# Optimization experiments

Hardware: AMD Instinct MI355X
Metric: run time of the kernel (lower is better)

Reference implementation:

```python
import jax, jax.numpy as jnp
import numpy as np
from jax import lax

B, T, D, K = 2, 4096, 128, 256


def setup_inputs() -> dict:
    key = jax.random.key(0)
    ks = jax.random.split(key, 5)
    s = 0.05
    return {
        "z": jax.random.normal(ks[0], (B, T, D), jnp.float32),
        "conv_kernel": jax.random.normal(ks[1], (K, 1, D), jnp.float32) * s,  # flax WIO depthwise
        "conv_bias": jnp.zeros((D,), jnp.float32),
        "Wq": jax.random.normal(ks[2], (D, D), jnp.float32) * s,
        "bq": jnp.zeros((D,), jnp.float32),
        "Wk": jax.random.normal(ks[3], (D, D), jnp.float32) * s,
        "bk": jnp.zeros((D,), jnp.float32),
        "Wo": jax.random.normal(ks[4], (D, D), jnp.float32) * s,
        "bo": jnp.zeros((D,), jnp.float32),
    }


def _sphere_norm(x):
    return x / jnp.maximum(jnp.linalg.norm(x, axis=-1, keepdims=True), 1e-8)


def reference(z, conv_kernel, conv_bias, Wq, bq, Wk, bk, Wo, bo):
    Bv, Tv, Dv = z.shape
    Kv = conv_kernel.shape[0]

    # Depthwise causal memory conv (flax nn.Conv, padding='CAUSAL', groups=D)
    memory_force = lax.conv_general_dilated(
        z, conv_kernel, window_strides=(1,), padding=[(Kv - 1, 0)],
        dimension_numbers=("NWC", "WIO", "NWC"), feature_group_count=Dv,
    ) + conv_bias

    # Keys are computed from the base point z once, shared across RK4 stages
    k_hat = _sphere_norm(z @ Wk + bk)  # [B,T,D]
    mask = jnp.tril(jnp.ones((Tv, Tv), z.dtype))  # causal mask

    def vector_field(z_curr):
        q_hat = _sphere_norm(z_curr @ Wq + bq)
        dots = jnp.einsum("btd,bsd->bts", q_hat, k_hat)  # [B,T,T]
        attn = jnp.sin(dots) * mask  # Kuramoto-style sin coupling, causal
        kuramoto = jnp.einsum("bts,bsd->btd", attn, k_hat) @ Wo + bo
        total = memory_force + kuramoto
        # project to tangent space of the sphere at z_curr
        return total - jnp.sum(total * z_curr, axis=-1, keepdims=True) * z_curr

    h = 1.0

    def retract(z_base, v):
        return _sphere_norm(z_base + v)

    k1 = vector_field(z)
    k2 = vector_field(retract(z, 0.5 * h * k1))
    k3 = vector_field(retract(z, 0.5 * h * k2))
    k4 = vector_field(retract(z, h * k3))
    v_final = (h / 6.0) * (k1 + 2 * k2 + 2 * k3 + k4)
    return retract(z, v_final)
```

## Files before the change

kernel.cpp:

```cpp
#include <hip/hip_runtime.h>
#include <hip/hip_bf16.h>

#define BB 2
#define TT 4096
#define DD 128
#define KK 256
#define NROW (BB*TT)
#define NELT (NROW*DD)

typedef _Float16 f16;
typedef __attribute__((ext_vector_type(8))) f16 half8;
typedef __attribute__((ext_vector_type(2))) __fp16 fp16x2;
typedef __attribute__((ext_vector_type(4))) float f32x4;
typedef __attribute__((ext_vector_type(16))) float f32x16;
typedef __attribute__((ext_vector_type(2))) int i32x2;
typedef __attribute__((ext_vector_type(4))) int i32x4;

__device__ __forceinline__ int pack2(float a, float b){
  fp16x2 h = __builtin_amdgcn_cvt_pkrtz(a, b);
  return __builtin_bit_cast(int, h);
}

__device__ __forceinline__ void stage_w_f16(int tid, const float* __restrict__ W, f16* Wh){
  #pragma unroll
  for (int it = 0; it < 8; it++){
    int idx = tid + it*256;
    f32x4 a = *(const f32x4*)(W + (size_t)idx*8);
    f32x4 b = *(const f32x4*)(W + (size_t)idx*8 + 4);
    half8 h;
    #pragma unroll
    for (int u = 0; u < 4; u++){ h[u] = (f16)a[u]; h[4+u] = (f16)b[u]; }
    *(half8*)(Wh + (size_t)idx*8) = h;
  }
}

__device__ __forceinline__ void proj_norm_rows(
    int tid, int r0,
    const float* __restrict__ src, const float* __restrict__ W, const float* __restrict__ bias,
    f16* __restrict__ dst, f16* __restrict__ dstT)
{
  __shared__ f16 Wh[DD*DD];
  __shared__ float zs[32*DD];
  stage_w_f16(tid, W, Wh);
  #pragma unroll
  for (int it = 0; it < 4; it++){
    int idx = tid + it*256;
    *(f32x4*)(zs + idx*4) = *(const f32x4*)(src + (size_t)r0*DD + idx*4);
  }
  __syncthreads();
  int c = tid & 15, rr = tid >> 4;
  float acc0[8], acc1[8];
  #pragma unroll
  for (int u = 0; u < 8; u++){ float bv = bias[c*8+u]; acc0[u] = bv; acc1[u] = bv; }
  const float* zr0 = zs + rr*DD;
  const float* zr1 = zs + (rr+16)*DD;
  #pragma unroll 4
  for (int i = 0; i < DD; i++){
    half8 wv = *(const half8*)(Wh + i*DD + c*8);
    float a0 = zr0[i], a1 = zr1[i];
    #pragma unroll
    for (int u = 0; u < 8; u++){
      float w = (float)wv[u];
      acc0[u] = fmaf(a0, w, acc0[u]);
      acc1[u] = fmaf(a1, w, acc1[u]);
    }
  }
  float s0 = 0.f, s1 = 0.f;
  #pragma unroll
  for (int u = 0; u < 8; u++){ s0 = fmaf(acc0[u], acc0[u], s0); s1 = fmaf(acc1[u], acc1[u], s1); }
  #pragma unroll
  for (int m = 1; m < 16; m <<= 1){ s0 += __shfl_xor(s0, m, 16); s1 += __shfl_xor(s1, m, 16); }
  float inv0 = 1.f / fmaxf(sqrtf(s0), 1e-8f);
  float inv1 = 1.f / fmaxf(sqrtf(s1), 1e-8f);
  half8 h0, h1;
  #pragma unroll
  for (int u = 0; u < 8; u++){ h0[u] = (f16)(acc0[u]*inv0); h1[u] = (f16)(acc1[u]*inv1); }
  int row0 = r0 + rr, row1 = row0 + 16;
  *(half8*)(dst + (size_t)row0*DD + c*8) = h0;
  *(half8*)(dst + (size_t)row1*DD + c*8) = h1;
  if (dstT){
    int b = row0 >> 12, t0 = row0 & 4095, t1 = row1 & 4095;
    #pragma unroll
    for (int u = 0; u < 8; u++){
      dstT[((size_t)b*DD + c*8 + u)*TT + t0] = h0[u];
      dstT[((size_t)b*DD + c*8 + u)*TT + t1] = h1[u];
    }
  }
}

__global__ __launch_bounds__(256) void k_prep(
    const float* __restrict__ z, const float* __restrict__ Wk, const float* __restrict__ bk,
    const float* __restrict__ ck, const float* __restrict__ cb,
    const float* __restrict__ Wq, const float* __restrict__ bq,
    f16* __restrict__ khb, f16* __restrict__ khT, f16* __restrict__ qhb,
    float* __restrict__ mf)
{
  int tid = threadIdx.x;
  if (blockIdx.x < 512){
    int bid = blockIdx.x;
    int d = tid & 127, tg = tid >> 7;
    int b = bid >> 8;
    int tbase = ((bid & 255) << 4) + tg*8;
    const float* zb = z + (size_t)b*TT*DD;
    float acc[8];
    #pragma unroll
    for (int j = 0; j < 8; j++) acc[j] = 0.f;
    float ckq[8];
    #pragma unroll
    for (int u = 0; u < 8; u++) ckq[u] = 0.f;
    int sstart = tbase - (KK-1);
    for (int ch = 0; ch < 33; ch++){
      #pragma unroll
      for (int u = 0; u < 8; u++){
        int base = ch*8 + u;
        int s = sstart + base;
        float zv = ((unsigned)s < (unsigned)TT && base < 263) ? zb[(size_t)s*DD + d] : 0.f;
        ckq[u] = (base < KK) ? ck[(size_t)base*DD + d] : 0.f;
        #pragma unroll
        for (int j = 0; j < 8; j++) acc[j] = fmaf(ckq[(u-j)&7], zv, acc[j]);
      }
    }
    float cbv = cb[d];
    #pragma unroll
    for (int j = 0; j < 8; j++)
      mf[((size_t)b*TT + tbase + j)*DD + d] = acc[j] + cbv;
  } else if (blockIdx.x < 768){
    proj_norm_rows(tid, (blockIdx.x - 512) * 32, z, Wk, bk, khb, khT);
  } else {
    proj_norm_rows(tid, (blockIdx.x - 768) * 32, z, Wq, bq, qhb, nullptr);
  }
}

#define QTILE 128
#define NQT3 (TT/QTILE)
#define NCHUNK 144

__global__ __launch_bounds__(256,2) void k_attn18(
    const f16* __restrict__ qhb, const f16* __restrict__ khb,
    const f16* __restrict__ khT, const float* __restrict__ Wo,
    f16* __restrict__ part)
{
  int bid = blockIdx.x;
  int b = bid / NCHUNK;
  int rem = bid - b*NCHUNK;
  int qt = 0, chunk = 0;
  #pragma unroll 1
  for (int j = NQT3-1; j >= 0; j--){
    int nch = (j + 4) >> 2;
    if (rem < nch){ qt = j; chunk = rem; break; }
    rem -= nch;
  }
  int kt0 = chunk * 8;
  int kt1 = min(kt0 + 7, 2*qt + 1);
  int t0 = qt * QTILE;

  __shared__ __align__(16) f16 KbD[2][64*136];
  __shared__ __align__(16) f16 KtD[2][128*72];

  int tid  = threadIdx.x;
  int w    = tid >> 6;
  int lane = tid & 63;
  int q31  = lane & 31;
  int hi   = lane >> 5;

  const f16* qg  = qhb + (size_t)b*TT*DD;
  const f16* kg  = khb + (size_t)b*TT*DD;
  const f16* ktg = khT + (size_t)b*DD*TT;

  int sb_r  = tid >> 4, sb_c = (tid & 15)*8;
  int st_r  = tid >> 3, st_c = (tid & 7)*8;

  int qrow_g = t0 + 32*w + q31;

  half8 qb[8];
  {
    const f16* qrow = qg + (size_t)qrow_g*DD + 8*hi;
    #pragma unroll
    for (int ks = 0; ks < 8; ks++) qb[ks] = *(const half8*)(qrow + 16*ks);
  }

  f32x16 acc[4];
  #pragma unroll
  for (int d = 0; d < 4; d++)
    #pragma unroll
    for (int i = 0; i < 16; i++) acc[d][i] = 0.f;

  half8 sKb[4], sKt[4];
  {
    int s0 = kt0 * 64;
    #pragma unroll
    for (int it = 0; it < 4; it++)
      sKb[it] = *(const half8*)(kg + (size_t)(s0 + sb_r + it*16)*DD + sb_c);
    #pragma unroll
    for (int it = 0; it < 4; it++)
      sKt[it] = *(const half8*)(ktg + (size_t)(st_r + it*32)*TT + s0 + st_c);
    #pragma unroll
    for (int it = 0; it < 4; it++)
      *(half8*)(&KbD[0][0] + (sb_r + it*16)*136 + sb_c) = sKb[it];
    #pragma unroll
    for (int it = 0; it < 4; it++)
      *(half8*)(&KtD[0][0] + (st_r + it*32)*72 + st_c) = sKt[it];
  }
  __syncthreads();

  #pragma unroll 1
  for (int kt = kt0; kt <= kt1; kt++){
    int cur = (kt - kt0) & 1;
    const f16* KbL = &KbD[cur][0];
    const f16* KtL = &KtD[cur][0];

    if (kt < kt1){
      int s0n = (kt+1) * 64;
      #pragma unroll
      for (int it = 0; it < 4; it++)
        sKb[it] = *(const half8*)(kg + (size_t)(s0n + sb_r + it*16)*DD + sb_c);
      #pragma unroll
      for (int it = 0; it < 4; it++)
        sKt[it] = *(const half8*)(ktg + (size_t)(st_r + it*32)*TT + s0n + st_c);
    }

    int s0 = kt * 64;
    f32x16 sa0, sa1;
    #pragma unroll
    for (int i = 0; i < 16; i++){ sa0[i] = 0.f; sa1[i] = 0.f; }
    #pragma unroll
    for (int ks = 0; ks < 8; ks++){
      half8 a0 = *(const half8*)(KbL + (q31)      *136 + 16*ks + 8*hi);
      half8 a1 = *(const half8*)(KbL + (32 + q31) *136 + 16*ks + 8*hi);
      sa0 = __builtin_amdgcn_mfma_f32_32x32x16_f16(a0, qb[ks], sa0, 0,0,0);
      sa1 = __builtin_amdgcn_mfma_f32_32x32x16_f16(a1, qb[ks], sa1, 0,0,0);
    }

    float p0v[16], p1v[16];
    #pragma unroll
    for (int r = 0; r < 16; r++){
      int kr = (r&3) + 8*(r>>2) + 4*hi;
      p0v[r] = (s0 + kr      <= qrow_g) ? __sinf(sa0[r]) : 0.f;
      p1v[r] = (s0 + 32 + kr <= qrow_g) ? __sinf(sa1[r]) : 0.f;
    }

    half8 pf[4];
    #pragma unroll
    for (int kb = 0; kb < 2; kb++){
      const float* pv = kb ? p1v : p0v;
      #pragma unroll
      for (int u = 0; u < 2; u++){
        int pl0 = pack2(pv[8*u+0], pv[8*u+1]);
        int pl1 = pack2(pv[8*u+2], pv[8*u+3]);
        int ph0 = pack2(pv[8*u+4], pv[8*u+5]);
        int ph1 = pack2(pv[8*u+6], pv[8*u+7]);
        int xl0 = __shfl_xor(pl0, 32);
        int xl1 = __shfl_xor(pl1, 32);
        int xh0 = __shfl_xor(ph0, 32);
        int xh1 = __shfl_xor(ph1, 32);
        i32x4 fr;
        fr[0] = hi ? xh0 : pl0;
        fr[1] = hi ? xh1 : pl1;
        fr[2] = hi ? ph0 : xl0;
        fr[3] = hi ? ph1 : xl1;
        pf[2*kb+u] = __builtin_bit_cast(half8, fr);
      }
    }

    #pragma unroll
    for (int s = 0; s < 4; s++){
      #pragma unroll
      for (int d0 = 0; d0 < 4; d0++){
        half8 bf = *(const half8*)(KtL + (32*d0 + q31)*72 + 16*s + 8*hi);
        acc[d0] = __builtin_amdgcn_mfma_f32_32x32x16_f16(bf, pf[s], acc[d0], 0,0,0);
      }
    }

    if (kt < kt1){
      f16* KbN = &KbD[cur^1][0];
      f16* KtN = &KtD[cur^1][0];
      #pragma unroll
      for (int it = 0; it < 4; it++)
        *(half8*)(KbN + (sb_r + it*16)*136 + sb_c) = sKb[it];
      #pragma unroll
      for (int it = 0; it < 4; it++)
        *(half8*)(KtN + (st_r + it*32)*72 + st_c) = sKt[it];
      __syncthreads();
    }
  }

  __syncthreads();
  f16* WoT = &KbD[0][0];
  {
    int j  = tid & 127;
    int ib = tid >> 7;
    #pragma unroll
    for (int u = 0; u < 8; u++){
      int i0 = ib*64 + u*8;
      half8 h;
      #pragma unroll
      for (int k = 0; k < 8; k++) h[k] = (f16)Wo[(size_t)(i0+k)*DD + j];
      *(half8*)(WoT + j*136 + i0) = h;
    }
  }
  half8 bO[8];
  #pragma unroll
  for (int d0 = 0; d0 < 4; d0++){
    #pragma unroll
    for (int m = 0; m < 2; m++){
      int pl0 = pack2(acc[d0][8*m+0], acc[d0][8*m+1]);
      int pl1 = pack2(acc[d0][8*m+2], acc[d0][8*m+3]);
      int ph0 = pack2(acc[d0][8*m+4], acc[d0][8*m+5]);
      int ph1 = pack2(acc[d0][8*m+6], acc[d0][8*m+7]);
      int xl0 = __shfl_xor(pl0, 32);
      int xl1 = __shfl_xor(pl1, 32);
      int xh0 = __shfl_xor(ph0, 32);
      int xh1 = __shfl_xor(ph1, 32);
      i32x4 fr;
      fr[0] = hi ? xh0 : pl0;
      fr[1] = hi ? xh1 : pl1;
      fr[2] = hi ? ph0 : xl0;
      fr[3] = hi ? ph1 : xl1;
      bO[2*d0+m] = __builtin_bit_cast(half8, fr);
    }
  }
  __syncthreads();

  f32x16 acc2[4];
  #pragma unroll
  for (int ob = 0; ob < 4; ob++)
    #pragma unroll
    for (int i = 0; i < 16; i++) acc2[ob][i] = 0.f;
  #pragma unroll
  for (int ks = 0; ks < 8; ks++){
    #pragma unroll
    for (int ob = 0; ob < 4; ob++){
      half8 af = *(const half8*)(WoT + (32*ob + q31)*136 + 16*ks + 8*hi);
      acc2[ob] = __builtin_amdgcn_mfma_f32_32x32x16_f16(af, bO[ks], acc2[ob], 0,0,0);
    }
  }

  f16* pb = part + (size_t)bid*(QTILE*DD) + (size_t)(32*w + q31)*DD;
  #pragma unroll
  for (int ob = 0; ob < 4; ob++){
    #pragma unroll
    for (int j = 0; j < 4; j++){
      i32x2 pw = { pack2(acc2[ob][4*j+0], acc2[ob][4*j+1]),
                   pack2(acc2[ob][4*j+2], acc2[ob][4*j+3]) };
      *(i32x2*)(pb + 32*ob + 8*j + 4*hi) = pw;
    }
  }
}

__global__ __launch_bounds__(256) void k_comb3(
    const float* __restrict__ z, const float* __restrict__ bo,
    const float* __restrict__ mf, const f16* __restrict__ part,
    const float* __restrict__ zin, float* __restrict__ zout,
    float* __restrict__ vsum, float* __restrict__ out,
    const float* __restrict__ Wq, const float* __restrict__ bq, f16* __restrict__ qhb,
    float wsum, float cretr, int first, int last)
{
  __shared__ f16 Wqh[DD*DD];
  __shared__ float As[32*DD];
  int tid = threadIdx.x;
  int r0 = blockIdx.x * 32;
  if (!last) stage_w_f16(tid, Wq, Wqh);
  {
    int b = r0 >> 12;
    int t = r0 & 4095;
    int qt = t >> 7;
    int ro = t & 127;
    int nc = (qt + 4) >> 2;
    int base = 0;
    #pragma unroll 1
    for (int j = NQT3-1; j > qt; j--) base += (j + 4) >> 2;
    size_t sb = ((size_t)b*NCHUNK + base)*(QTILE*DD) + (size_t)ro*DD;
    #pragma unroll
    for (int it = 0; it < 2; it++){
      int idx = tid + it*256;
      const f16* s = part + sb + (size_t)idx*8;
      float a[8];
      {
        half8 v = *(const half8*)(s);
        #pragma unroll
        for (int u = 0; u < 8; u++) a[u] = (float)v[u];
      }
      for (int cc = 1; cc < nc; cc++){
        half8 v = *(const half8*)(s + (size_t)cc*(QTILE*DD));
        #pragma unroll
        for (int u = 0; u < 8; u++) a[u] += (float)v[u];
      }
      f32x4 o0v = {a[0],a[1],a[2],a[3]}, o1v = {a[4],a[5],a[6],a[7]};
      *(f32x4*)(As + idx*8) = o0v;
      *(f32x4*)(As + idx*8 + 4) = o1v;
    }
  }
  __syncthreads();
  int c = tid & 15, rr = tid >> 4;
  float kur0[8], kur1[8];
  {
    f32x4 k0a = *(const f32x4*)(As + rr*DD + c*8);
    f32x4 k0b = *(const f32x4*)(As + rr*DD + c*8 + 4);
    f32x4 k1a = *(const f32x4*)(As + (rr+16)*DD + c*8);
    f32x4 k1b = *(const f32x4*)(As + (rr+16)*DD + c*8 + 4);
    #pragma unroll
    for (int u = 0; u < 4; u++){
      float bva = bo[c*8+u], bvb = bo[c*8+4+u];
      kur0[u] = k0a[u] + bva; kur0[4+u] = k0b[u] + bvb;
      kur1[u] = k1a[u] + bva; kur1[4+u] = k1b[u] + bvb;
    }
  }
  size_t o0 = (size_t)(r0+rr)*DD + c*8;
  size_t o1 = (size_t)(r0+rr+16)*DD + c*8;
  float tot0[8], tot1[8], zi0[8], zi1[8];
  {
    f32x4 m0a = *(const f32x4*)(mf + o0), m0b = *(const f32x4*)(mf + o0 + 4);
    f32x4 m1a = *(const f32x4*)(mf + o1), m1b = *(const f32x4*)(mf + o1 + 4);
    f32x4 z0a = *(const f32x4*)(zin + o0), z0b = *(const f32x4*)(zin + o0 + 4);
    f32x4 z1a = *(const f32x4*)(zin + o1), z1b = *(const f32x4*)(zin + o1 + 4);
    #pragma unroll
    for (int u = 0; u < 4; u++){
      tot0[u] = m0a[u] + kur0[u]; tot0[4+u] = m0b[u] + kur0[4+u];
      tot1[u] = m1a[u] + kur1[u]; tot1[4+u] = m1b[u] + kur1[4+u];
      zi0[u] = z0a[u]; zi0[4+u] = z0b[u];
      zi1[u] = z1a[u]; zi1[4+u] = z1b[u];
    }
  }
  float p0 = 0.f, p1 = 0.f;
  #pragma unroll
  for (int u = 0; u < 8; u++){ p0 = fmaf(tot0[u], zi0[u], p0); p1 = fmaf(tot1[u], zi1[u], p1); }
  #pragma unroll
  for (int m = 1; m < 16; m <<= 1){ p0 += __shfl_xor(p0, m, 16); p1 += __shfl_xor(p1, m, 16); }
  float ki0[8], ki1[8], vs0[8], vs1[8];
  #pragma unroll
  for (int u = 0; u < 8; u++){
    ki0[u] = tot0[u] - p0 * zi0[u];
    ki1[u] = tot1[u] - p1 * zi1[u];
  }
  if (first){
    #pragma unroll
    for (int u = 0; u < 8; u++){ vs0[u] = wsum*ki0[u]; vs1[u] = wsum*ki1[u]; }
  } else {
    f32x4 v0a = *(const f32x4*)(vsum + o0), v0b = *(const f32x4*)(vsum + o0 + 4);
    f32x4 v1a = *(const f32x4*)(vsum + o1), v1b = *(const f32x4*)(vsum + o1 + 4);
    #pragma unroll
    for (int u = 0; u < 4; u++){
      vs0[u] = fmaf(wsum, ki0[u], v0a[u]); vs0[4+u] = fmaf(wsum, ki0[4+u], v0b[u]);
      vs1[u] = fmaf(wsum, ki1[u], v1a[u]); vs1[4+u] = fmaf(wsum, ki1[4+u], v1b[u]);
    }
  }
  if (!last){
    f32x4 va = {vs0[0],vs0[1],vs0[2],vs0[3]}, vb = {vs0[4],vs0[5],vs0[6],vs0[7]};
    f32x4 vc = {vs1[0],vs1[1],vs1[2],vs1[3]}, vd = {vs1[4],vs1[5],vs1[6],vs1[7]};
    *(f32x4*)(vsum + o0) = va; *(f32x4*)(vsum + o0 + 4) = vb;
    *(f32x4*)(vsum + o1) = vc; *(f32x4*)(vsum + o1 + 4) = vd;
  }
  float nz0[8], nz1[8];
  {
    f32x4 z0a = *(const f32x4*)(z + o0), z0b = *(const f32x4*)(z + o0 + 4);
    f32x4 z1a = *(const f32x4*)(z + o1), z1b = *(const f32x4*)(z + o1 + 4);
    #pragma unroll
    for (int u = 0; u < 4; u++){
      float d0a = last ? vs0[u]*(1.f/6.f)   : cretr*ki0[u];
      float d0b = last ? vs0[4+u]*(1.f/6.f) : cretr*ki0[4+u];
      float d1a = last ? vs1[u]*(1.f/6.f)   : cretr*ki1[u];
      float d1b = last ? vs1[4+u]*(1.f/6.f) : cretr*ki1[4+u];
      nz0[u] = z0a[u] + d0a; nz0[4+u] = z0b[u] + d0b;
      nz1[u] = z1a[u] + d1a; nz1[4+u] = z1b[u] + d1b;
    }
  }
  float n0 = 0.f, n1 = 0.f;
  #pragma unroll
  for (int u = 0; u < 8; u++){ n0 = fmaf(nz0[u], nz0[u], n0); n1 = fmaf(nz1[u], nz1[u], n1); }
  #pragma unroll
  for (int m = 1; m < 16; m <<= 1){ n0 += __shfl_xor(n0, m, 16); n1 += __shfl_xor(n1, m, 16); }
  float i0 = 1.f / fmaxf(sqrtf(n0), 1e-8f);
  float i1 = 1.f / fmaxf(sqrtf(n1), 1e-8f);
  float* dst = last ? out : zout;
  f32x4 ra = {nz0[0]*i0, nz0[1]*i0, nz0[2]*i0, nz0[3]*i0};
  f32x4 rb = {nz0[4]*i0, nz0[5]*i0, nz0[6]*i0, nz0[7]*i0};
  f32x4 rc = {nz1[0]*i1, nz1[1]*i1, nz1[2]*i1, nz1[3]*i1};
  f32x4 rd = {nz1[4]*i1, nz1[5]*i1, nz1[6]*i1, nz1[7]*i1};
  *(f32x4*)(dst + o0) = ra; *(f32x4*)(dst + o0 + 4) = rb;
  *(f32x4*)(dst + o1) = rc; *(f32x4*)(dst + o1 + 4) = rd;

  if (!last){
    __syncthreads();
    *(f32x4*)(As + rr*DD + c*8)          = ra;
    *(f32x4*)(As + rr*DD + c*8 + 4)      = rb;
    *(f32x4*)(As + (rr+16)*DD + c*8)     = rc;
    *(f32x4*)(As + (rr+16)*DD + c*8 + 4) = rd;
    __syncthreads();
    float q0[8], q1[8];
    #pragma unroll
    for (int u = 0; u < 8; u++){ float bv = bq[c*8+u]; q0[u] = bv; q1[u] = bv; }
    const float* qr0 = As + rr*DD;
    const float* qr1 = As + (rr+16)*DD;
    #pragma unroll 4
    for (int i = 0; i < DD; i++){
      half8 wv = *(const half8*)(Wqh + i*DD + c*8);
      float a0 = qr0[i], a1 = qr1[i];
      #pragma unroll
      for (int u = 0; u < 8; u++){
        float w = (float)wv[u];
        q0[u] = fmaf(a0, w, q0[u]);
        q1[u] = fmaf(a1, w, q1[u]);
      }
    }
    float s0 = 0.f, s1 = 0.f;
    #pragma unroll
    for (int u = 0; u < 8; u++){ s0 = fmaf(q0[u], q0[u], s0); s1 = fmaf(q1[u], q1[u], s1); }
    #pragma unroll
    for (int m = 1; m < 16; m <<= 1){ s0 += __shfl_xor(s0, m, 16); s1 += __shfl_xor(s1, m, 16); }
    float qi0 = 1.f / fmaxf(sqrtf(s0), 1e-8f);
    float qi1 = 1.f / fmaxf(sqrtf(s1), 1e-8f);
    half8 h0, h1;
    #pragma unroll
    for (int u = 0; u < 8; u++){ h0[u] = (f16)(q0[u]*qi0); h1[u] = (f16)(q1[u]*qi1); }
    *(half8*)(qhb + (size_t)(r0+rr)*DD + c*8)    = h0;
    *(half8*)(qhb + (size_t)(r0+rr+16)*DD + c*8) = h1;
  }
}

extern "C" void kernel_launch(void* const* d_in, const int* in_sizes, int n_in,
                              void* d_out, int out_size, void* d_ws, size_t ws_size,
                              hipStream_t stream) {
  const float* z  = (const float*)d_in[0];
  const float* ck = (const float*)d_in[1];
  const float* cb = (const float*)d_in[2];
  const float* Wq = (const float*)d_in[3];
  const float* bq = (const float*)d_in[4];
  const float* Wk = (const float*)d_in[5];
  const float* bk = (const float*)d_in[6];
  const float* Wo = (const float*)d_in[7];
  const float* bo = (const float*)d_in[8];
  float* out = (float*)d_out;

  float* mf   = (float*)d_ws;
  float* zc   = mf   + NELT;
  float* vsum = zc   + NELT;
  f16*   khb  = (f16*)(vsum + NELT);
  f16*   khT  = khb  + NELT;
  f16*   qhb  = khT  + NELT;
  f16*   part = qhb  + NELT;

  k_prep<<<1024, 256, 0, stream>>>(z, Wk, bk, ck, cb, Wq, bq, khb, khT, qhb, mf);

  const float wv[4] = {1.f, 2.f, 2.f, 1.f};
  const float cv[4] = {0.5f, 0.5f, 1.f, 0.f};
  for (int st = 0; st < 4; st++){
    const float* zcur = (st == 0) ? z : zc;
    k_attn18<<<BB*NCHUNK, 256, 0, stream>>>(qhb, khb, khT, Wo, part);
    k_comb3 <<<NROW/32, 256, 0, stream>>>(z, bo, mf, part, zcur, zc, vsum, out,
                                          Wq, bq, qhb, wv[st], cv[st], st == 0, st == 3);
  }
}
```

Before: 268.2 us.

## Halve attention key-chunk size, store fp32 partials, widen combine blocks to 512 threads

```diff
diff --git a/kernel.cpp b/kernel.cpp
--- a/kernel.cpp
+++ b/kernel.cpp
@@ -133,12 +133,12 @@
 
 #define QTILE 128
 #define NQT3 (TT/QTILE)
-#define NCHUNK 144
-
-__global__ __launch_bounds__(256,2) void k_attn18(
+#define NCHUNK 272
+
+__global__ __launch_bounds__(256,2) void k_attn19(
     const f16* __restrict__ qhb, const f16* __restrict__ khb,
     const f16* __restrict__ khT, const float* __restrict__ Wo,
-    f16* __restrict__ part)
+    float* __restrict__ part)
 {
   int bid = blockIdx.x;
   int b = bid / NCHUNK;
@@ -146,12 +146,12 @@
   int qt = 0, chunk = 0;
   #pragma unroll 1
   for (int j = NQT3-1; j >= 0; j--){
-    int nch = (j + 4) >> 2;
+    int nch = (2*j + 5) >> 2;
     if (rem < nch){ qt = j; chunk = rem; break; }
     rem -= nch;
   }
-  int kt0 = chunk * 8;
-  int kt1 = min(kt0 + 7, 2*qt + 1);
+  int kt0 = chunk * 4;
+  int kt1 = min(kt0 + 3, 2*qt + 1);
   int t0 = qt * QTILE;
 
   __shared__ __align__(16) f16 KbD[2][64*136];
@@ -335,21 +335,20 @@
     }
   }
 
-  f16* pb = part + (size_t)bid*(QTILE*DD) + (size_t)(32*w + q31)*DD;
+  float* pb = part + (size_t)bid*(QTILE*DD) + (size_t)(32*w + q31)*DD;
   #pragma unroll
   for (int ob = 0; ob < 4; ob++){
     #pragma unroll
     for (int j = 0; j < 4; j++){
-      i32x2 pw = { pack2(acc2[ob][4*j+0], acc2[ob][4*j+1]),
-                   pack2(acc2[ob][4*j+2], acc2[ob][4*j+3]) };
-      *(i32x2*)(pb + 32*ob + 8*j + 4*hi) = pw;
-    }
-  }
-}
-
-__global__ __launch_bounds__(256) void k_comb3(
+      f32x4 v = {acc2[ob][4*j+0], acc2[ob][4*j+1], acc2[ob][4*j+2], acc2[ob][4*j+3]};
+      *(f32x4*)(pb + 32*ob + 8*j + 4*hi) = v;
+    }
+  }
+}
+
+__global__ __launch_bounds__(512) void k_comb4(
     const float* __restrict__ z, const float* __restrict__ bo,
-    const float* __restrict__ mf, const f16* __restrict__ part,
+    const float* __restrict__ mf, const float* __restrict__ part,
     const float* __restrict__ zin, float* __restrict__ zout,
     float* __restrict__ vsum, float* __restrict__ out,
     const float* __restrict__ Wq, const float* __restrict__ bq, f16* __restrict__ qhb,
@@ -359,161 +358,135 @@
   __shared__ float As[32*DD];
   int tid = threadIdx.x;
   int r0 = blockIdx.x * 32;
-  if (!last) stage_w_f16(tid, Wq, Wqh);
+  if (!last){
+    #pragma unroll
+    for (int it = 0; it < 4; it++){
+      int idx = tid + it*512;
+      f32x4 a = *(const f32x4*)(Wq + (size_t)idx*8);
+      f32x4 b = *(const f32x4*)(Wq + (size_t)idx*8 + 4);
+      half8 h;
+      #pragma unroll
+      for (int u = 0; u < 4; u++){ h[u] = (f16)a[u]; h[4+u] = (f16)b[u]; }
+      *(half8*)(Wqh + (size_t)idx*8) = h;
+    }
+  }
   {
     int b = r0 >> 12;
     int t = r0 & 4095;
     int qt = t >> 7;
     int ro = t & 127;
-    int nc = (qt + 4) >> 2;
+    int nc = (2*qt + 5) >> 2;
     int base = 0;
     #pragma unroll 1
-    for (int j = NQT3-1; j > qt; j--) base += (j + 4) >> 2;
+    for (int j = NQT3-1; j > qt; j--) base += (2*j + 5) >> 2;
     size_t sb = ((size_t)b*NCHUNK + base)*(QTILE*DD) + (size_t)ro*DD;
-    #pragma unroll
-    for (int it = 0; it < 2; it++){
-      int idx = tid + it*256;
-      const f16* s = part + sb + (size_t)idx*8;
-      float a[8];
-      {
-        half8 v = *(const half8*)(s);
-        #pragma unroll
-        for (int u = 0; u < 8; u++) a[u] = (float)v[u];
-      }
-      for (int cc = 1; cc < nc; cc++){
-        half8 v = *(const half8*)(s + (size_t)cc*(QTILE*DD));
-        #pragma unroll
-        for (int u = 0; u < 8; u++) a[u] += (float)v[u];
-      }
-      f32x4 o0v = {a[0],a[1],a[2],a[3]}, o1v = {a[4],a[5],a[6],a[7]};
-      *(f32x4*)(As + idx*8) = o0v;
-      *(f32x4*)(As + idx*8 + 4) = o1v;
-    }
+    const float* s = part + sb + (size_t)tid*8;
+    f32x4 a0 = *(const f32x4*)(s);
+    f32x4 a1 = *(const f32x4*)(s + 4);
+    for (int cc = 1; cc < nc; cc++){
+      const float* sc = s + (size_t)cc*(QTILE*DD);
+      a0 += *(const f32x4*)(sc);
+      a1 += *(const f32x4*)(sc + 4);
+    }
+    *(f32x4*)(As + (size_t)tid*8) = a0;
+    *(f32x4*)(As + (size_t)tid*8 + 4) = a1;
   }
   __syncthreads();
   int c = tid & 15, rr = tid >> 4;
-  float kur0[8], kur1[8];
+  float kur0[8];
   {
     f32x4 k0a = *(const f32x4*)(As + rr*DD + c*8);
     f32x4 k0b = *(const f32x4*)(As + rr*DD + c*8 + 4);
-    f32x4 k1a = *(const f32x4*)(As + (rr+16)*DD + c*8);
-    f32x4 k1b = *(const f32x4*)(As + (rr+16)*DD + c*8 + 4);
     #pragma unroll
     for (int u = 0; u < 4; u++){
-      float bva = bo[c*8+u], bvb = bo[c*8+4+u];
-      kur0[u] = k0a[u] + bva; kur0[4+u] = k0b[u] + bvb;
-      kur1[u] = k1a[u] + bva; kur1[4+u] = k1b[u] + bvb;
+      kur0[u] = k0a[u] + bo[c*8+u];
+      kur0[4+u] = k0b[u] + bo[c*8+4+u];
     }
   }
   size_t o0 = (size_t)(r0+rr)*DD + c*8;
-  size_t o1 = (size_t)(r0+rr+16)*DD + c*8;
-  float tot0[8], tot1[8], zi0[8], zi1[8];
+  float tot0[8], zi0[8];
   {
     f32x4 m0a = *(const f32x4*)(mf + o0), m0b = *(const f32x4*)(mf + o0 + 4);
-    f32x4 m1a = *(const f32x4*)(mf + o1), m1b = *(const f32x4*)(mf + o1 + 4);
     f32x4 z0a = *(const f32x4*)(zin + o0), z0b = *(const f32x4*)(zin + o0 + 4);
-    f32x4 z1a = *(const f32x4*)(zin + o1), z1b = *(const f32x4*)(zin + o1 + 4);
     #pragma unroll
     for (int u = 0; u < 4; u++){
       tot0[u] = m0a[u] + kur0[u]; tot0[4+u] = m0b[u] + kur0[4+u];
-      tot1[u] = m1a[u] + kur1[u]; tot1[4+u] = m1b[u] + kur1[4+u];
       zi0[u] = z0a[u]; zi0[4+u] = z0b[u];
-      zi1[u] = z1a[u]; zi1[4+u] = z1b[u];
-    }
-  }
-  float p0 = 0.f, p1 = 0.f;
-  #pragma unroll
-  for (int u = 0; u < 8; u++){ p0 = fmaf(tot0[u], zi0[u], p0); p1 = fmaf(tot1[u], zi1[u], p1); }
-  #pragma unroll
-  for (int m = 1; m < 16; m <<= 1){ p0 += __shfl_xor(p0, m, 16); p1 += __shfl_xor(p1, m, 16); }
-  float ki0[8], ki1[8], vs0[8], vs1[8];
+    }
+  }
+  float p0 = 0.f;
+  #pragma unroll
+  for (int u = 0; u < 8; u++){ p0 = fmaf(tot0[u], zi0[u], p0); }
+  #pragma unroll
+  for (int m = 1; m < 16; m <<= 1){ p0 += __shfl_xor(p0, m, 16); }
+  float ki0[8], vs0[8];
   #pragma unroll
   for (int u = 0; u < 8; u++){
     ki0[u] = tot0[u] - p0 * zi0[u];
-    ki1[u] = tot1[u] - p1 * zi1[u];
   }
   if (first){
     #pragma unroll
-    for (int u = 0; u < 8; u++){ vs0[u] = wsum*ki0[u]; vs1[u] = wsum*ki1[u]; }
+    for (int u = 0; u < 8; u++){ vs0[u] = wsum*ki0[u]; }
   } else {
     f32x4 v0a = *(const f32x4*)(vsum + o0), v0b = *(const f32x4*)(vsum + o0 + 4);
-    f32x4 v1a = *(const f32x4*)(vsum + o1), v1b = *(const f32x4*)(vsum + o1 + 4);
     #pragma unroll
     for (int u = 0; u < 4; u++){
       vs0[u] = fmaf(wsum, ki0[u], v0a[u]); vs0[4+u] = fmaf(wsum, ki0[4+u], v0b[u]);
-      vs1[u] = fmaf(wsum, ki1[u], v1a[u]); vs1[4+u] = fmaf(wsum, ki1[4+u], v1b[u]);
     }
   }
   if (!last){
     f32x4 va = {vs0[0],vs0[1],vs0[2],vs0[3]}, vb = {vs0[4],vs0[5],vs0[6],vs0[7]};
-    f32x4 vc = {vs1[0],vs1[1],vs1[2],vs1[3]}, vd = {vs1[4],vs1[5],vs1[6],vs1[7]};
     *(f32x4*)(vsum + o0) = va; *(f32x4*)(vsum + o0 + 4) = vb;
-    *(f32x4*)(vsum + o1) = vc; *(f32x4*)(vsum + o1 + 4) = vd;
-  }
-  float nz0[8], nz1[8];
+  }
+  float nz0[8];
   {
     f32x4 z0a = *(const f32x4*)(z + o0), z0b = *(const f32x4*)(z + o0 + 4);
-    f32x4 z1a = *(const f32x4*)(z + o1), z1b = *(const f32x4*)(z + o1 + 4);
     #pragma unroll
     for (int u = 0; u < 4; u++){
       float d0a = last ? vs0[u]*(1.f/6.f)   : cretr*ki0[u];
       float d0b = last ? vs0[4+u]*(1.f/6.f) : cretr*ki0[4+u];
-      float d1a = last ? vs1[u]*(1.f/6.f)   : cretr*ki1[u];
-      float d1b = last ? vs1[4+u]*(1.f/6.f) : cretr*ki1[4+u];
       nz0[u] = z0a[u] + d0a; nz0[4+u] = z0b[u] + d0b;
-      nz1[u] = z1a[u] + d1a; nz1[4+u] = z1b[u] + d1b;
-    }
-  }
-  float n0 = 0.f, n1 = 0.f;
-  #pragma unroll
-  for (int u = 0; u < 8; u++){ n0 = fmaf(nz0[u], nz0[u], n0); n1 = fmaf(nz1[u], nz1[u], n1); }
-  #pragma unroll
-  for (int m = 1; m < 16; m <<= 1){ n0 += __shfl_xor(n0, m, 16); n1 += __shfl_xor(n1, m, 16); }
+    }
+  }
+  float n0 = 0.f;
+  #pragma unroll
+  for (int u = 0; u < 8; u++){ n0 = fmaf(nz0[u], nz0[u], n0); }
+  #pragma unroll
+  for (int m = 1; m < 16; m <<= 1){ n0 += __shfl_xor(n0, m, 16); }
   float i0 = 1.f / fmaxf(sqrtf(n0), 1e-8f);
-  float i1 = 1.f / fmaxf(sqrtf(n1), 1e-8f);
   float* dst = last ? out : zout;
   f32x4 ra = {nz0[0]*i0, nz0[1]*i0, nz0[2]*i0, nz0[3]*i0};
   f32x4 rb = {nz0[4]*i0, nz0[5]*i0, nz0[6]*i0, nz0[7]*i0};
-  f32x4 rc = {nz1[0]*i1, nz1[1]*i1, nz1[2]*i1, nz1[3]*i1};
-  f32x4 rd = {nz1[4]*i1, nz1[5]*i1, nz1[6]*i1, nz1[7]*i1};
   *(f32x4*)(dst + o0) = ra; *(f32x4*)(dst + o0 + 4) = rb;
-  *(f32x4*)(dst + o1) = rc; *(f32x4*)(dst + o1 + 4) = rd;
 
   if (!last){
     __syncthreads();
-    *(f32x4*)(As + rr*DD + c*8)          = ra;
-    *(f32x4*)(As + rr*DD + c*8 + 4)      = rb;
-    *(f32x4*)(As + (rr+16)*DD + c*8)     = rc;
-    *(f32x4*)(As + (rr+16)*DD + c*8 + 4) = rd;
+    *(f32x4*)(As + rr*DD + c*8)     = ra;
+    *(f32x4*)(As + rr*DD + c*8 + 4) = rb;
     __syncthreads();
-    float q0[8], q1[8];
-    #pragma unroll
-    for (int u = 0; u < 8; u++){ float bv = bq[c*8+u]; q0[u] = bv; q1[u] = bv; }
+    float q0[8];
+    #pragma unroll
+    for (int u = 0; u < 8; u++){ q0[u] = bq[c*8+u]; }
     const float* qr0 = As + rr*DD;
-    const float* qr1 = As + (rr+16)*DD;
     #pragma unroll 4
     for (int i = 0; i < DD; i++){
       half8 wv = *(const half8*)(Wqh + i*DD + c*8);
-      float a0 = qr0[i], a1 = qr1[i];
+      float a0 = qr0[i];
       #pragma unroll
       for (int u = 0; u < 8; u++){
-        float w = (float)wv[u];
-        q0[u] = fmaf(a0, w, q0[u]);
-        q1[u] = fmaf(a1, w, q1[u]);
+        q0[u] = fmaf(a0, (float)wv[u], q0[u]);
       }
     }
-    float s0 = 0.f, s1 = 0.f;
-    #pragma unroll
-    for (int u = 0; u < 8; u++){ s0 = fmaf(q0[u], q0[u], s0); s1 = fmaf(q1[u], q1[u], s1); }
-    #pragma unroll
-    for (int m = 1; m < 16; m <<= 1){ s0 += __shfl_xor(s0, m, 16); s1 += __shfl_xor(s1, m, 16); }
+    float s0 = 0.f;
+    #pragma unroll
+    for (int u = 0; u < 8; u++){ s0 = fmaf(q0[u], q0[u], s0); }
+    #pragma unroll
+    for (int m = 1; m < 16; m <<= 1){ s0 += __shfl_xor(s0, m, 16); }
     float qi0 = 1.f / fmaxf(sqrtf(s0), 1e-8f);
-    float qi1 = 1.f / fmaxf(sqrtf(s1), 1e-8f);
-    half8 h0, h1;
-    #pragma unroll
-    for (int u = 0; u < 8; u++){ h0[u] = (f16)(q0[u]*qi0); h1[u] = (f16)(q1[u]*qi1); }
-    *(half8*)(qhb + (size_t)(r0+rr)*DD + c*8)    = h0;
-    *(half8*)(qhb + (size_t)(r0+rr+16)*DD + c*8) = h1;
+    half8 h0;
+    #pragma unroll
+    for (int u = 0; u < 8; u++){ h0[u] = (f16)(q0[u]*qi0); }
+    *(half8*)(qhb + (size_t)(r0+rr)*DD + c*8) = h0;
   }
 }
 
@@ -537,7 +510,7 @@
   f16*   khb  = (f16*)(vsum + NELT);
   f16*   khT  = khb  + NELT;
   f16*   qhb  = khT  + NELT;
-  f16*   part = qhb  + NELT;
+  float* part = (float*)(qhb + NELT);
 
   k_prep<<<1024, 256, 0, stream>>>(z, Wk, bk, ck, cb, Wq, bq, khb, khT, qhb, mf);
 
@@ -545,8 +518,8 @@
   const float cv[4] = {0.5f, 0.5f, 1.f, 0.f};
   for (int st = 0; st < 4; st++){
     const float* zcur = (st == 0) ? z : zc;
-    k_attn18<<<BB*NCHUNK, 256, 0, stream>>>(qhb, khb, khT, Wo, part);
-    k_comb3 <<<NROW/32, 256, 0, stream>>>(z, bo, mf, part, zcur, zc, vsum, out,
+    k_attn19<<<BB*NCHUNK, 256, 0, stream>>>(qhb, khb, khT, Wo, part);
+    k_comb4 <<<NROW/32, 512, 0, stream>>>(z, bo, mf, part, zcur, zc, vsum, out,
                                           Wq, bq, qhb, wv[st], cv[st], st == 0, st == 3);
   }
 }
```

Result: slower. 283.5 us (+5.7%).
